# Kernel tuning notes

Measured on AMD Instinct MI355X. Metric: run time of the kernel, lower is better.

Reference implementation:

```python
import jax, jax.numpy as jnp
import numpy as np

B, T, D = 16, 2048, 64


def setup_inputs() -> dict:
    key = jax.random.key(0)
    kq, kk, kv, kb = jax.random.split(key, 4)
    q = jax.random.normal(kq, (B, T, D), dtype=jnp.float32)
    k = jax.random.normal(kk, (B, T, D), dtype=jnp.float32)
    v = jax.random.normal(kv, (B, T, D), dtype=jnp.float32)
    add_attn = jax.random.normal(kb, (B, T, T), dtype=jnp.float32)
    return {"q": q, "k": k, "v": v, "add_attn": add_attn}


def reference(q, k, v, add_attn):
    # scale = 1/sqrt(head_dim), the standard value passed by callers
    scale = 1.0 / jnp.sqrt(jnp.asarray(q.shape[-1], dtype=q.dtype))
    # [B, T, T] attention logits: bmm(q, k^T) * scale + additive bias
    attn = jnp.einsum('btd,bsd->bts', q, k) * scale + add_attn
    # softmax over keys (dim=2); dropout p=0.0 is identity
    attn = jax.nn.softmax(attn, axis=2)
    # [B, T, D] weighted values
    output = jnp.einsum('bts,bsd->btd', attn, v)
    return (output, attn)
```

## Files before the change

kernel.cpp:

```cpp
#include <hip/hip_runtime.h>
#include <stdint.h>

#define NB 16
#define NT 2048
#define ND 64

typedef __attribute__((ext_vector_type(8))) short bf16x8;
typedef __attribute__((ext_vector_type(4))) float f32x4;
typedef __attribute__((ext_vector_type(4))) _Float16 f16x4;
typedef __attribute__((ext_vector_type(2))) _Float16 f16x2;

__device__ __forceinline__ unsigned short f2bf(float f) {
    union { float f; unsigned u; } v; v.f = f;
    unsigned r = v.u + 0x7fffu + ((v.u >> 16) & 1u);
    return (unsigned short)(r >> 16);
}
__device__ __forceinline__ unsigned short f2h(float f) {
    union { _Float16 h; unsigned short u; } v; v.h = (_Float16)f; return v.u;
}

__global__ __launch_bounds__(256) void prep_k(const float* __restrict__ Q,
                                              const float* __restrict__ K,
                                              const float* __restrict__ V,
                                              unsigned short* __restrict__ qbf,
                                              unsigned short* __restrict__ kbf,
                                              unsigned short* __restrict__ vt)
{
    const size_t i = (size_t)blockIdx.x * 256 + threadIdx.x;
    const int which = blockIdx.y;
    if (which == 2) {
        float4 v4 = ((const float4*)V)[i];
        const int d4 = (int)(i & 15);
        const int t  = (int)((i >> 4) & (NT - 1));
        const int b  = (int)(i >> 15);
        unsigned short* base = vt + ((size_t)b * ND + d4 * 4) * NT + t;
        base[0]      = f2h(v4.x);
        base[NT]     = f2h(v4.y);
        base[2 * NT] = f2h(v4.z);
        base[3 * NT] = f2h(v4.w);
    } else {
        const float4* src = (which == 0) ? (const float4*)Q : (const float4*)K;
        unsigned short* dst = (which == 0) ? qbf : kbf;
        float4 v4 = src[i];
        union { unsigned short s[4]; unsigned long long ll; } u;
        u.s[0] = f2bf(v4.x); u.s[1] = f2bf(v4.y);
        u.s[2] = f2bf(v4.z); u.s[3] = f2bf(v4.w);
        *(unsigned long long*)(dst + 4 * i) = u.ll;
    }
}

__global__ __launch_bounds__(256, 3)
void attn_onepass(const unsigned short* __restrict__ qbf,
                  const unsigned short* __restrict__ kbf,
                  const unsigned short* __restrict__ vt,
                  const float* __restrict__ Bias,
                  float* __restrict__ Out,
                  float* __restrict__ Attn)
{
    const int b = blockIdx.y, q0 = blockIdx.x * 16;
    const int tid = threadIdx.x, w = tid >> 6, lane = tid & 63;
    const int n = lane & 15, qd = lane >> 4;
    const int kw0 = w * 512;

    __shared__ float s_rs[4][16];
    __shared__ float s_o[4 * 16 * 68];

    const unsigned short* qp = qbf + ((size_t)(b * NT + q0 + n)) * ND + qd * 8;
    const bf16x8 qf0 = *(const bf16x8*)qp;
    const bf16x8 qf1 = *(const bf16x8*)(qp + 32);
    const float* Bb = Bias + ((size_t)b * NT + q0 + n) * NT;
    float* Ab = Attn + ((size_t)b * NT + q0 + n) * NT;
    const unsigned short* vtb = vt + (size_t)b * ND * NT + (size_t)n * NT;

    f16x2 ev[32][2];
    float rs = 0.f;
#pragma unroll
    for (int t = 0; t < 32; ++t) {
        const int key0 = kw0 + 16 * t;
        const unsigned short* kp = kbf + ((size_t)(b * NT + key0 + n)) * ND + qd * 8;
        bf16x8 kf0 = *(const bf16x8*)kp;
        bf16x8 kf1 = *(const bf16x8*)(kp + 32);
        f32x4 acc = {0.f, 0.f, 0.f, 0.f};
        acc = __builtin_amdgcn_mfma_f32_16x16x32_bf16(kf0, qf0, acc, 0, 0, 0);
        acc = __builtin_amdgcn_mfma_f32_16x16x32_bf16(kf1, qf1, acc, 0, 0, 0);
        float4 bs = *(const float4*)(Bb + key0 + qd * 4);
        float e0 = __expf(__builtin_fmaf(acc[0], 0.125f, bs.x - 2.0f));
        float e1 = __expf(__builtin_fmaf(acc[1], 0.125f, bs.y - 2.0f));
        float e2 = __expf(__builtin_fmaf(acc[2], 0.125f, bs.z - 2.0f));
        float e3 = __expf(__builtin_fmaf(acc[3], 0.125f, bs.w - 2.0f));
        ev[t][0][0] = (_Float16)e0; ev[t][0][1] = (_Float16)e1;
        ev[t][1][0] = (_Float16)e2; ev[t][1][1] = (_Float16)e3;
        rs += (e0 + e1) + (e2 + e3);
    }

    rs += __shfl_xor(rs, 16, 64);
    rs += __shfl_xor(rs, 32, 64);
    if (lane < 16) s_rs[w][lane] = rs;
    __syncthreads();
    const float tot = (s_rs[0][n] + s_rs[1][n]) + (s_rs[2][n] + s_rs[3][n]);
    const float inv = 1.0f / tot;

    f32x4 oacc[4];
#pragma unroll
    for (int dt = 0; dt < 4; ++dt) oacc[dt] = (f32x4){0.f, 0.f, 0.f, 0.f};

#pragma unroll
    for (int t = 0; t < 32; ++t) {
        const int key0 = kw0 + 16 * t;
        float p0 = (float)ev[t][0][0] * inv;
        float p1 = (float)ev[t][0][1] * inv;
        float p2 = (float)ev[t][1][0] * inv;
        float p3 = (float)ev[t][1][1] * inv;
        float4 s; s.x = p0; s.y = p1; s.z = p2; s.w = p3;
        *(float4*)(Ab + key0 + qd * 4) = s;
        f16x4 pf;
        pf[0] = (_Float16)p0; pf[1] = (_Float16)p1;
        pf[2] = (_Float16)p2; pf[3] = (_Float16)p3;
        const unsigned short* vp = vtb + key0 + qd * 4;
#pragma unroll
        for (int dt = 0; dt < 4; ++dt) {
            f16x4 vf = *(const f16x4*)(const void*)(vp + (size_t)dt * 16 * NT);
            oacc[dt] = __builtin_amdgcn_mfma_f32_16x16x16f16(vf, pf, oacc[dt], 0, 0, 0);
        }
    }

#pragma unroll
    for (int dt = 0; dt < 4; ++dt) {
        float4 t4; t4.x = oacc[dt][0]; t4.y = oacc[dt][1];
        t4.z = oacc[dt][2]; t4.w = oacc[dt][3];
        *(float4*)&s_o[(w * 16 + n) * 68 + dt * 16 + qd * 4] = t4;
    }
    __syncthreads();
    {
        const int row = tid >> 4, d4 = (tid & 15) * 4;
        float4 o0 = *(const float4*)&s_o[(0 * 16 + row) * 68 + d4];
        float4 o1 = *(const float4*)&s_o[(1 * 16 + row) * 68 + d4];
        float4 o2 = *(const float4*)&s_o[(2 * 16 + row) * 68 + d4];
        float4 o3 = *(const float4*)&s_o[(3 * 16 + row) * 68 + d4];
        float4 o;
        o.x = (o0.x + o1.x) + (o2.x + o3.x);
        o.y = (o0.y + o1.y) + (o2.y + o3.y);
        o.z = (o0.z + o1.z) + (o2.z + o3.z);
        o.w = (o0.w + o1.w) + (o2.w + o3.w);
        *(float4*)(Out + ((size_t)b * NT + q0 + row) * ND + d4) = o;
    }
}

__device__ __forceinline__ bf16x8 pack8(float4 a, float4 b) {
    union { unsigned short s[8]; bf16x8 v; } u;
    u.s[0] = f2bf(a.x); u.s[1] = f2bf(a.y); u.s[2] = f2bf(a.z); u.s[3] = f2bf(a.w);
    u.s[4] = f2bf(b.x); u.s[5] = f2bf(b.y); u.s[6] = f2bf(b.z); u.s[7] = f2bf(b.w);
    return u.v;
}
__global__ __launch_bounds__(256, 2)
void attn_fused(const float* __restrict__ Q, const float* __restrict__ K,
                const float* __restrict__ V, const float* __restrict__ Bias,
                float* __restrict__ Out, float* __restrict__ Attn)
{
    const int b  = blockIdx.y;
    const int q0 = blockIdx.x * 16;
    const int tid  = threadIdx.x;
    const int w    = tid >> 6;
    const int lane = tid & 63;
    const int n  = lane & 15;
    const int qd = lane >> 4;
    const int kw0 = w * 512;
    __shared__ float s_rs[4][16];
    __shared__ __align__(16) unsigned char s_rp[4][16 * 80];
    const float* Qb = Q + ((size_t)b * NT + q0) * ND;
    const float* Kb = K + (size_t)b * NT * ND;
    const float* Vb = V + (size_t)b * NT * ND;
    const float* Bb = Bias + ((size_t)b * NT + q0) * NT;
    float* Ab = Attn + ((size_t)b * NT + q0) * NT;
    float* Ob = Out  + ((size_t)b * NT + q0) * ND;
    bf16x8 qf0, qf1;
    {
        const float* qp = Qb + n * ND + qd * 8;
        qf0 = pack8(*(const float4*)qp,        *(const float4*)(qp + 4));
        qf1 = pack8(*(const float4*)(qp + 32), *(const float4*)(qp + 36));
    }
    float ev[32][4];
    float rs = 0.f;
#pragma unroll
    for (int t = 0; t < 32; ++t) {
        const int key0 = kw0 + 16 * t;
        const float* kp = Kb + (size_t)(key0 + n) * ND + qd * 8;
        bf16x8 kf0 = pack8(*(const float4*)kp,        *(const float4*)(kp + 4));
        bf16x8 kf1 = pack8(*(const float4*)(kp + 32), *(const float4*)(kp + 36));
        f32x4 acc = {0.f, 0.f, 0.f, 0.f};
        acc = __builtin_amdgcn_mfma_f32_16x16x32_bf16(kf0, qf0, acc, 0, 0, 0);
        acc = __builtin_amdgcn_mfma_f32_16x16x32_bf16(kf1, qf1, acc, 0, 0, 0);
        float4 bs = *(const float4*)(Bb + (size_t)n * NT + key0 + qd * 4);
        float e0 = __expf(acc[0] * 0.125f + bs.x);
        float e1 = __expf(acc[1] * 0.125f + bs.y);
        float e2 = __expf(acc[2] * 0.125f + bs.z);
        float e3 = __expf(acc[3] * 0.125f + bs.w);
        ev[t][0] = e0; ev[t][1] = e1; ev[t][2] = e2; ev[t][3] = e3;
        rs += (e0 + e1) + (e2 + e3);
    }
    rs += __shfl_xor(rs, 16, 64);
    rs += __shfl_xor(rs, 32, 64);
    if (lane < 16) s_rs[w][lane] = rs;
    __syncthreads();
    const float tot = (s_rs[0][n] + s_rs[1][n]) + (s_rs[2][n] + s_rs[3][n]);
    const float inv = 1.0f / tot;
    f32x4 oacc[4];
#pragma unroll
    for (int dt = 0; dt < 4; ++dt) oacc[dt] = (f32x4){0.f, 0.f, 0.f, 0.f};
    unsigned char* rp = &s_rp[w][0];
#pragma unroll
    for (int c = 0; c < 16; ++c) {
        const int kbase = kw0 + 32 * c;
#pragma unroll
        for (int tt = 0; tt < 2; ++tt) {
            const int t = 2 * c + tt;
            float p0 = ev[t][0] * inv;
            float p1 = ev[t][1] * inv;
            float p2 = ev[t][2] * inv;
            float p3 = ev[t][3] * inv;
            float4 pv; pv.x = p0; pv.y = p1; pv.z = p2; pv.w = p3;
            *(float4*)(Ab + (size_t)n * NT + kbase + 16 * tt + qd * 4) = pv;
            union { unsigned short s[4]; unsigned long long ll; } pu;
            pu.s[0] = f2bf(p0); pu.s[1] = f2bf(p1);
            pu.s[2] = f2bf(p2); pu.s[3] = f2bf(p3);
            *(unsigned long long*)(rp + n * 80 + (16 * tt + 4 * qd) * 2) = pu.ll;
        }
        __syncthreads();
        bf16x8 pf;
        {
            union { uint4 u; bf16x8 v; } uu;
            uu.u = *(const uint4*)(rp + n * 80 + qd * 16);
            pf = uu.v;
        }
#pragma unroll
        for (int dt = 0; dt < 4; ++dt) {
            const int d = dt * 16 + n;
            const float* vp = Vb + (size_t)(kbase + qd * 8) * ND + d;
            float4 va, vb4;
            va.x  = vp[0];   va.y  = vp[64];  va.z  = vp[128]; va.w  = vp[192];
            vb4.x = vp[256]; vb4.y = vp[320]; vb4.z = vp[384]; vb4.w = vp[448];
            bf16x8 vf = pack8(va, vb4);
            oacc[dt] = __builtin_amdgcn_mfma_f32_16x16x32_bf16(vf, pf, oacc[dt], 0, 0, 0);
        }
        __syncthreads();
    }
#pragma unroll
    for (int dt = 0; dt < 4; ++dt)
#pragma unroll
        for (int r = 0; r < 4; ++r)
            atomicAdd(Ob + (size_t)n * ND + dt * 16 + qd * 4 + r, oacc[dt][r]);
}

extern "C" void kernel_launch(void* const* d_in, const int* in_sizes, int n_in,
                              void* d_out, int out_size, void* d_ws, size_t ws_size,
                              hipStream_t stream)
{
    const float* q    = (const float*)d_in[0];
    const float* k    = (const float*)d_in[1];
    const float* v    = (const float*)d_in[2];
    const float* bias = (const float*)d_in[3];
    float* out  = (float*)d_out;
    float* attn = out + (size_t)NB * NT * ND;

    const size_t elems = (size_t)NB * NT * ND;
    const size_t need  = 3 * elems * 2;

    if (ws_size >= need) {
        unsigned short* qbf = (unsigned short*)d_ws;
        unsigned short* kbf = qbf + elems;
        unsigned short* vtb = kbf + elems;
        prep_k<<<dim3((unsigned)(elems / 4 / 256), 3), 256, 0, stream>>>(q, k, v, qbf, kbf, vtb);
        attn_onepass<<<dim3(NT / 16, NB), 256, 0, stream>>>(qbf, kbf, vtb, bias, out, attn);
    } else {
        hipMemsetAsync(out, 0, (size_t)NB * NT * ND * sizeof(float), stream);
        dim3 grid(NT / 16, NB);
        attn_fused<<<grid, 256, 0, stream>>>(q, k, v, bias, out, attn);
    }
}
```

Before: 298.8 us.

## Software-prefetch K, bias and V tiles and defer softmax normalization to output

Adds register double-buffering: K fragments are prefetched two tiles ahead, bias four tiles ahead, and V fragments one 32-key step ahead, so global loads overlap the MFMA and exp work. The PV MFMA now consumes unnormalized fp16 exponentials, and the 1/sum factor is applied once to the output accumulator instead of per probability. This removes per-element rescale and conversion work. The cost is higher register pressure, which may reduce occupancy.

```diff
diff --git a/kernel.cpp b/kernel.cpp
--- a/kernel.cpp
+++ b/kernel.cpp
@@ -8,7 +8,6 @@
 typedef __attribute__((ext_vector_type(8))) short bf16x8;
 typedef __attribute__((ext_vector_type(4))) float f32x4;
 typedef __attribute__((ext_vector_type(4))) _Float16 f16x4;
-typedef __attribute__((ext_vector_type(2))) _Float16 f16x2;
 
 __device__ __forceinline__ unsigned short f2bf(float f) {
     union { float f; unsigned u; } v; v.f = f;
@@ -72,25 +71,53 @@
     float* Ab = Attn + ((size_t)b * NT + q0 + n) * NT;
     const unsigned short* vtb = vt + (size_t)b * ND * NT + (size_t)n * NT;
 
-    f16x2 ev[32][2];
+    f16x4 ev[32];
+    float4 bb[4];
+    bf16x8 kb0[2], kb1[2];
+#pragma unroll
+    for (int i = 0; i < 4; ++i)
+        bb[i] = *(const float4*)(Bb + kw0 + 16 * i + qd * 4);
+#pragma unroll
+    for (int i = 0; i < 2; ++i) {
+        const unsigned short* kp = kbf + ((size_t)(b * NT + kw0 + 16 * i + n)) * ND + qd * 8;
+        kb0[i] = *(const bf16x8*)kp;
+        kb1[i] = *(const bf16x8*)(kp + 32);
+    }
+
     float rs = 0.f;
 #pragma unroll
     for (int t = 0; t < 32; ++t) {
-        const int key0 = kw0 + 16 * t;
-        const unsigned short* kp = kbf + ((size_t)(b * NT + key0 + n)) * ND + qd * 8;
-        bf16x8 kf0 = *(const bf16x8*)kp;
-        bf16x8 kf1 = *(const bf16x8*)(kp + 32);
+        const bf16x8 kf0 = kb0[t & 1];
+        const bf16x8 kf1 = kb1[t & 1];
+        const float4 bs = bb[t & 3];
+        if (t + 2 < 32) {
+            const unsigned short* kp =
+                kbf + ((size_t)(b * NT + kw0 + 16 * (t + 2) + n)) * ND + qd * 8;
+            kb0[t & 1] = *(const bf16x8*)kp;
+            kb1[t & 1] = *(const bf16x8*)(kp + 32);
+        }
+        if (t + 4 < 32)
+            bb[t & 3] = *(const float4*)(Bb + kw0 + 16 * (t + 4) + qd * 4);
         f32x4 acc = {0.f, 0.f, 0.f, 0.f};
         acc = __builtin_amdgcn_mfma_f32_16x16x32_bf16(kf0, qf0, acc, 0, 0, 0);
         acc = __builtin_amdgcn_mfma_f32_16x16x32_bf16(kf1, qf1, acc, 0, 0, 0);
-        float4 bs = *(const float4*)(Bb + key0 + qd * 4);
         float e0 = __expf(__builtin_fmaf(acc[0], 0.125f, bs.x - 2.0f));
         float e1 = __expf(__builtin_fmaf(acc[1], 0.125f, bs.y - 2.0f));
         float e2 = __expf(__builtin_fmaf(acc[2], 0.125f, bs.z - 2.0f));
         float e3 = __expf(__builtin_fmaf(acc[3], 0.125f, bs.w - 2.0f));
-        ev[t][0][0] = (_Float16)e0; ev[t][0][1] = (_Float16)e1;
-        ev[t][1][0] = (_Float16)e2; ev[t][1][1] = (_Float16)e3;
+        union { _Float16 h[4]; f16x4 v; } u;
+        u.h[0] = (_Float16)e0; u.h[1] = (_Float16)e1;
+        u.h[2] = (_Float16)e2; u.h[3] = (_Float16)e3;
+        ev[t] = u.v;
         rs += (e0 + e1) + (e2 + e3);
+    }
+
+    f16x4 vc0[4], vc1[4];
+#pragma unroll
+    for (int dt = 0; dt < 4; ++dt) {
+        const unsigned short* vp = vtb + kw0 + qd * 4 + (size_t)dt * 16 * NT;
+        vc0[dt] = *(const f16x4*)(const void*)vp;
+        vc1[dt] = *(const f16x4*)(const void*)(vp + 16);
     }
 
     rs += __shfl_xor(rs, 16, 64);
@@ -105,29 +132,41 @@
     for (int dt = 0; dt < 4; ++dt) oacc[dt] = (f32x4){0.f, 0.f, 0.f, 0.f};
 
 #pragma unroll
-    for (int t = 0; t < 32; ++t) {
-        const int key0 = kw0 + 16 * t;
-        float p0 = (float)ev[t][0][0] * inv;
-        float p1 = (float)ev[t][0][1] * inv;
-        float p2 = (float)ev[t][1][0] * inv;
-        float p3 = (float)ev[t][1][1] * inv;
-        float4 s; s.x = p0; s.y = p1; s.z = p2; s.w = p3;
-        *(float4*)(Ab + key0 + qd * 4) = s;
-        f16x4 pf;
-        pf[0] = (_Float16)p0; pf[1] = (_Float16)p1;
-        pf[2] = (_Float16)p2; pf[3] = (_Float16)p3;
-        const unsigned short* vp = vtb + key0 + qd * 4;
+    for (int tp = 0; tp < 16; ++tp) {
+        const int key0 = kw0 + 32 * tp;
+        f16x4 va0[4], va1[4];
+#pragma unroll
+        for (int dt = 0; dt < 4; ++dt) { va0[dt] = vc0[dt]; va1[dt] = vc1[dt]; }
+        if (tp + 1 < 16) {
+#pragma unroll
+            for (int dt = 0; dt < 4; ++dt) {
+                const unsigned short* vp =
+                    vtb + key0 + 32 + qd * 4 + (size_t)dt * 16 * NT;
+                vc0[dt] = *(const f16x4*)(const void*)vp;
+                vc1[dt] = *(const f16x4*)(const void*)(vp + 16);
+            }
+        }
+        const f16x4 e0v = ev[2 * tp];
+        const f16x4 e1v = ev[2 * tp + 1];
+        float4 s0, s1;
+        s0.x = (float)e0v[0] * inv; s0.y = (float)e0v[1] * inv;
+        s0.z = (float)e0v[2] * inv; s0.w = (float)e0v[3] * inv;
+        s1.x = (float)e1v[0] * inv; s1.y = (float)e1v[1] * inv;
+        s1.z = (float)e1v[2] * inv; s1.w = (float)e1v[3] * inv;
+        *(float4*)(Ab + key0 + qd * 4) = s0;
+        *(float4*)(Ab + key0 + 16 + qd * 4) = s1;
 #pragma unroll
         for (int dt = 0; dt < 4; ++dt) {
-            f16x4 vf = *(const f16x4*)(const void*)(vp + (size_t)dt * 16 * NT);
-            oacc[dt] = __builtin_amdgcn_mfma_f32_16x16x16f16(vf, pf, oacc[dt], 0, 0, 0);
+            oacc[dt] = __builtin_amdgcn_mfma_f32_16x16x16f16(va0[dt], e0v, oacc[dt], 0, 0, 0);
+            oacc[dt] = __builtin_amdgcn_mfma_f32_16x16x16f16(va1[dt], e1v, oacc[dt], 0, 0, 0);
         }
     }
 
 #pragma unroll
     for (int dt = 0; dt < 4; ++dt) {
-        float4 t4; t4.x = oacc[dt][0]; t4.y = oacc[dt][1];
-        t4.z = oacc[dt][2]; t4.w = oacc[dt][3];
+        float4 t4;
+        t4.x = oacc[dt][0] * inv; t4.y = oacc[dt][1] * inv;
+        t4.z = oacc[dt][2] * inv; t4.w = oacc[dt][3] * inv;
         *(float4*)&s_o[(w * 16 + n) * 68 + dt * 16 + qd * 4] = t4;
     }
     __syncthreads();
```

Result: faster. 282.6 us (-5.4%).
